# Kernel optimization log

Measured on AMD Instinct MI355X. Metric: run time of the kernel, lower is better.

## Reference

```python
import jax, jax.numpy as jnp
import numpy as np

N, E, IN_DIM, HID, H, D = 50000, 800000, 1280, 256, 4, 64  # gat_out_dim = H*D = HID
NEG_SLOPE = 0.2


def setup_inputs() -> dict:
    key = jax.random.key(0)
    ks = jax.random.split(key, 20)

    def lin(k, fi, fo):
        return (jax.random.normal(k, (fi, fo), jnp.float32) / np.float32(np.sqrt(fi)))

    inp = {
        "x": jax.random.normal(ks[0], (N, IN_DIM), jnp.float32),
        "edge_index": jax.random.randint(ks[1], (2, E), 0, N, dtype=jnp.int32),
        "enc_W": lin(ks[2], IN_DIM, HID), "enc_b": jnp.zeros((HID,), jnp.float32),
        "Wl0": lin(ks[3], HID, H * D), "bl0": jnp.zeros((H * D,), jnp.float32),
        "Wr0": lin(ks[4], HID, H * D), "br0": jnp.zeros((H * D,), jnp.float32),
        "att0": jax.random.normal(ks[5], (H, D), jnp.float32) / np.float32(np.sqrt(D)),
        "bias0": jnp.zeros((H * D,), jnp.float32),
        "Wl1": lin(ks[6], HID, H * D), "bl1": jnp.zeros((H * D,), jnp.float32),
        "Wr1": lin(ks[7], HID, H * D), "br1": jnp.zeros((H * D,), jnp.float32),
        "att1": jax.random.normal(ks[8], (H, D), jnp.float32) / np.float32(np.sqrt(D)),
        "bias1": jnp.zeros((H * D,), jnp.float32),
        "clf_W": lin(ks[9], HID, 1), "clf_b": jnp.zeros((1,), jnp.float32),
    }
    return inp


def gatv2_layer(x, src, dst, Wl, bl, Wr, br, att, bias):
    # x: [N, HID]; src/dst: [E'] with self-loops already appended
    xl = (x @ Wl + bl).reshape(N, H, D)  # source transform
    xr = (x @ Wr + br).reshape(N, H, D)  # target transform
    e = jax.nn.leaky_relu(xl[src] + xr[dst], NEG_SLOPE)   # [E', H, D]
    logits = jnp.einsum('ehd,hd->eh', e, att)              # [E', H]
    # segment softmax over destination nodes (every node has a self-loop)
    m = jax.ops.segment_max(logits, dst, num_segments=N)   # [N, H]
    a = jnp.exp(logits - m[dst])
    denom = jax.ops.segment_sum(a, dst, num_segments=N)
    alpha = a / (denom[dst] + 1e-16)                       # [E', H]
    out = jax.ops.segment_sum(xl[src] * alpha[:, :, None], dst, num_segments=N)
    out = out.reshape(N, H * D) + bias
    out = out + x  # residual (in_dim == out_features -> identity residual); dropout is eval-mode no-op
    return jax.nn.elu(out), alpha


def reference(x, edge_index, enc_W, enc_b, Wl0, bl0, Wr0, br0, att0, bias0,
              Wl1, bl1, Wr1, br1, att1, bias1, clf_W, clf_b):
    # add self loops (PyG GATv2Conv default)
    loops = jnp.arange(N, dtype=edge_index.dtype)
    src = jnp.concatenate([edge_index[0], loops])
    dst = jnp.concatenate([edge_index[1], loops])

    h = x @ enc_W + enc_b                                  # node encoder [N, HID]
    h, alpha0 = gatv2_layer(h, src, dst, Wl0, bl0, Wr0, br0, att0, bias0)
    h, alpha1 = gatv2_layer(h, src, dst, Wl1, bl1, Wr1, br1, att1, bias1)
    preds = (h @ clf_W + clf_b).squeeze(-1)                # [N]
    return preds, alpha0, alpha1
```

## Files before the change

kernel.cpp:

```cpp
#include <hip/hip_runtime.h>
#include <hip/hip_bf16.h>
#include <math.h>

#define N_NODES 50000
#define E_EDGES 800000
#define EP (E_EDGES + N_NODES)
#define IN_DIM 1280
#define HID 256
#define NHEAD 4
#define DHEAD 64
#define NEG_SLOPE 0.2f

typedef unsigned short ushort_t;
typedef __attribute__((ext_vector_type(8))) short short8;
typedef __attribute__((ext_vector_type(4))) float floatx4;

__device__ __forceinline__ void split_bf16(float x, ushort_t& hi, ushort_t& lo) {
  unsigned u = __float_as_uint(x);
  hi = (ushort_t)(u >> 16);
  float rem = x - __uint_as_float(u & 0xFFFF0000u);
  lo = (ushort_t)(__float_as_uint(rem) >> 16);
}

__device__ __forceinline__ void gload_lds16(const void* g, void* l) {
  __builtin_amdgcn_global_load_lds(
      (const __attribute__((address_space(1))) unsigned int*)g,
      (__attribute__((address_space(3))) unsigned int*)l, 16, 0, 0);
}


__global__ void hist_kernel(const int* __restrict__ ei, int* __restrict__ deg) {
  int e = blockIdx.x * blockDim.x + threadIdx.x;
  if (e >= EP) return;
  int dst = (e < E_EDGES) ? ei[E_EDGES + e] : (e - E_EDGES);
  atomicAdd(&deg[dst], 1);
}

__global__ __launch_bounds__(1024) void scan_kernel(int* __restrict__ dc, int* __restrict__ row_ptr) {
  __shared__ int wsum[16];
  int tid = threadIdx.x;
  int lane = tid & 63;
  int wid = tid >> 6;
  int running = 0;
  if (tid == 0) row_ptr[0] = 0;
  for (int base = 0; base < N_NODES; base += 1024) {
    int i = base + tid;
    int v = (i < N_NODES) ? dc[i] : 0;
    int s = v;
    #pragma unroll
    for (int off = 1; off < 64; off <<= 1) {
      int t = __shfl_up(s, off);
      if (lane >= off) s += t;
    }
    if (lane == 63) wsum[wid] = s;
    __syncthreads();
    if (wid == 0 && lane < 16) {
      int w = wsum[lane];
      #pragma unroll
      for (int off = 1; off < 16; off <<= 1) {
        int t = __shfl_up(w, off);
        if (lane >= off) w += t;
      }
      wsum[lane] = w;
    }
    __syncthreads();
    int woff = (wid > 0) ? wsum[wid - 1] : 0;
    int incl = running + woff + s;
    if (i < N_NODES) {
      row_ptr[i + 1] = incl;
      dc[i] = incl - v;
    }
    running += wsum[15];
    __syncthreads();
  }
}

__global__ void scatter_kernel(const int* __restrict__ ei, int* __restrict__ cursor,
                               int2* __restrict__ csr_se) {
  int e = blockIdx.x * blockDim.x + threadIdx.x;
  if (e >= EP) return;
  int src, dst;
  if (e < E_EDGES) { src = ei[e]; dst = ei[E_EDGES + e]; }
  else             { src = dst = e - E_EDGES; }
  int pos = atomicAdd(&cursor[dst], 1);
  csr_se[pos] = make_int2(src, e);
}

#define ENC_ELEMS (IN_DIM * HID)
#define LYR_ELEMS (HID * HID)
__global__ void wsplit_all(const float* __restrict__ enc_W,
                           const float* __restrict__ Wl0, const float* __restrict__ Wr0,
                           const float* __restrict__ Wl1, const float* __restrict__ Wr1,
                           ushort_t* __restrict__ encPh, ushort_t* __restrict__ encPl,
                           ushort_t* __restrict__ P0h, ushort_t* __restrict__ P0l,
                           ushort_t* __restrict__ P1h, ushort_t* __restrict__ P1l) {
  int idx = blockIdx.x * blockDim.x + threadIdx.x;
  const float* W; ushort_t *Ph, *Pl; int NcT, colOff, r;
  if (idx < ENC_ELEMS) {
    W = enc_W; Ph = encPh; Pl = encPl; NcT = HID; colOff = 0; r = idx;
  } else {
    int q = idx - ENC_ELEMS;
    int mId = q >> 16;
    if (mId >= 4) return;
    r = q & 0xFFFF;
    W  = (mId == 0) ? Wl0 : (mId == 1) ? Wr0 : (mId == 2) ? Wl1 : Wr1;
    Ph = (mId < 2) ? P0h : P1h;
    Pl = (mId < 2) ? P0l : P1l;
    NcT = 512; colOff = (mId & 1) * 256;
  }
  int k = r >> 8, n = r & 255;
  ushort_t hi, lo;
  split_bf16(W[r], hi, lo);
  size_t pi = ((size_t)(k >> 3) * NcT + colOff + n) * 8 + (k & 7);
  Ph[pi] = hi;
  Pl[pi] = lo;
}

__device__ __forceinline__ void split_store16(const float* va, ushort_t* dAh,
                                              ushort_t* dAl, int awoff) {
  #pragma unroll
  for (int hh = 0; hh < 2; ++hh) {
    short8 hv, lv;
    #pragma unroll
    for (int i = 0; i < 8; ++i) {
      ushort_t hi, lo;
      split_bf16(va[hh * 8 + i], hi, lo);
      hv[i] = (short)hi; lv[i] = (short)lo;
    }
    *(short8*)&dAh[awoff + hh * 8] = hv;
    *(short8*)&dAl[awoff + hh * 8] = lv;
  }
}

__global__ __launch_bounds__(256, 2) void gemm128(const float* __restrict__ A,
                                                  const ushort_t* __restrict__ Bh,
                                                  const ushort_t* __restrict__ Bl,
                                                  const float* __restrict__ bias_l,
                                                  const float* __restrict__ bias_r,
                                                  float* __restrict__ C_l,
                                                  float* __restrict__ C_r,
                                                  int M, int K, int NcT, int Nsplit) {
  __shared__ ushort_t sAh[2][128 * 40];
  __shared__ ushort_t sAl[2][128 * 40];
  __shared__ ushort_t sBh[2][128 * 32];
  __shared__ ushort_t sBl[2][128 * 32];

  const int P = NcT >> 7;
  const int plog = (P == 2) ? 1 : 2;
  const int id = blockIdx.x;
  const int xcd = id & 7;
  const int kk = id >> 3;
  const int cpan = kk & (P - 1);
  const int Rhi = kk >> plog;
  const int R = (Rhi << 3) + xcd;
  const int MBp = (M + 127) >> 7;
  if (R >= MBp) return;

  const int tid = threadIdx.x;
  const int lane = tid & 63;
  const int w = tid >> 6;
  const int wm = w >> 1, wn = w & 1;
  const int bm = R * 128;
  const int bn = cpan * 128;
  const int r = lane & 15, q = lane >> 4;

  floatx4 acc[4][4];
  #pragma unroll
  for (int i = 0; i < 4; ++i)
    #pragma unroll
    for (int j = 0; j < 4; ++j) acc[i][j] = (floatx4)(0.0f);

  const int arow = tid >> 1, achunk = tid & 1;
  int ag = bm + arow; if (ag >= M) ag = M - 1;
  const float* aptr = A + (size_t)ag * K + achunk * 16;
  const int awoff = arow * 40 + achunk * 16;

  const int e0 = tid, e1 = tid + 256;
  const size_t b0base = ((size_t)(e0 >> 7) * NcT + bn + (e0 & 127)) * 8;
  const size_t b1base = ((size_t)(e1 >> 7) * NcT + bn + (e1 & 127)) * 8;

  const int nt = K >> 5;

  {
    gload_lds16(Bh + b0base, &sBh[0][e0 * 8]);
    gload_lds16(Bh + b1base, &sBh[0][e1 * 8]);
    gload_lds16(Bl + b0base, &sBl[0][e0 * 8]);
    gload_lds16(Bl + b1base, &sBl[0][e1 * 8]);
    float va[16];
    *(float4*)&va[0]  = *(const float4*)(aptr + 0);
    *(float4*)&va[4]  = *(const float4*)(aptr + 4);
    *(float4*)&va[8]  = *(const float4*)(aptr + 8);
    *(float4*)&va[12] = *(const float4*)(aptr + 12);
    split_store16(va, sAh[0], sAl[0], awoff);
  }
  __syncthreads();

  int cur = 0;
  for (int t = 0; t < nt; ++t) {
    const bool has_next = (t + 1 < nt);
    float va[16];
    if (has_next) {
      const int k0n = (t + 1) << 5;
      *(float4*)&va[0]  = *(const float4*)(aptr + k0n + 0);
      *(float4*)&va[4]  = *(const float4*)(aptr + k0n + 4);
      *(float4*)&va[8]  = *(const float4*)(aptr + k0n + 8);
      *(float4*)&va[12] = *(const float4*)(aptr + k0n + 12);
      size_t kadd = (size_t)(k0n >> 3) * NcT * 8;
      gload_lds16(Bh + b0base + kadd, &sBh[cur ^ 1][e0 * 8]);
      gload_lds16(Bh + b1base + kadd, &sBh[cur ^ 1][e1 * 8]);
      gload_lds16(Bl + b0base + kadd, &sBl[cur ^ 1][e0 * 8]);
      gload_lds16(Bl + b1base + kadd, &sBl[cur ^ 1][e1 * 8]);
    }

    short8 ah[4], al[4];
    #pragma unroll
    for (int i = 0; i < 4; ++i) {
      int off = (wm * 64 + i * 16 + r) * 40 + q * 8;
      ah[i] = *(const short8*)&sAh[cur][off];
      al[i] = *(const short8*)&sAl[cur][off];
    }
    #pragma unroll
    for (int j = 0; j < 4; ++j) {
      int off = (q * 128 + wn * 64 + j * 16 + r) * 8;
      short8 bh = *(const short8*)&sBh[cur][off];
      short8 bl = *(const short8*)&sBl[cur][off];
      #pragma unroll
      for (int i = 0; i < 4; ++i) {
        acc[i][j] = __builtin_amdgcn_mfma_f32_16x16x32_bf16(ah[i], bh, acc[i][j], 0, 0, 0);
        acc[i][j] = __builtin_amdgcn_mfma_f32_16x16x32_bf16(ah[i], bl, acc[i][j], 0, 0, 0);
        acc[i][j] = __builtin_amdgcn_mfma_f32_16x16x32_bf16(al[i], bh, acc[i][j], 0, 0, 0);
      }
    }

    if (has_next) split_store16(va, sAh[cur ^ 1], sAl[cur ^ 1], awoff);

    __syncthreads();
    cur ^= 1;
  }

  #pragma unroll
  for (int j = 0; j < 4; ++j) {
    int cg = bn + wn * 64 + j * 16 + r;
    bool sec = cg >= Nsplit;
    int cc = sec ? cg - Nsplit : cg;
    float bv = sec ? bias_r[cc] : bias_l[cc];
    float* Cb = sec ? C_r : C_l;
    #pragma unroll
    for (int i = 0; i < 4; ++i) {
      int row0 = bm + wm * 64 + i * 16 + q * 4;
      #pragma unroll
      for (int rr = 0; rr < 4; ++rr) {
        int row = row0 + rr;
        if (row < M) Cb[(size_t)row * HID + cc] = acc[i][j][rr] + bv;
      }
    }
  }
}

__global__ __launch_bounds__(256) void gat_layer(const float* __restrict__ xl,
                                                 const float* __restrict__ xr,
                                                 float* h_inout,
                                                 const float* __restrict__ att,
                                                 const float* __restrict__ bias,
                                                 const int* __restrict__ row_ptr,
                                                 const int2* __restrict__ csr_se,
                                                 float* __restrict__ logits_ws,
                                                 float* __restrict__ alpha_out,
                                                 const float* __restrict__ clf_W,
                                                 const float* __restrict__ clf_b,
                                                 float* __restrict__ preds) {
  int node = blockIdx.x * 4 + (threadIdx.x >> 6);
  int l = threadIdx.x & 63;
  int hgrp = l >> 4;
  int r0 = row_ptr[node];
  int r1 = row_ptr[node + 1];

  float4 xr4 = *(const float4*)(xr + (size_t)node * HID + l * 4);
  float4 at4 = *(const float4*)(att + l * 4);

  float mA = -INFINITY, mB = -INFINITY;
  float dA = 0.f, dB = 0.f;
  float4 aA = make_float4(0.f, 0.f, 0.f, 0.f);
  float4 aB = make_float4(0.f, 0.f, 0.f, 0.f);

  auto process = [&](const float4& v, int j, float& m, float& den, float4& acc) {
    float t0 = v.x + xr4.x; t0 = (t0 > 0.f) ? t0 : NEG_SLOPE * t0;
    float t1 = v.y + xr4.y; t1 = (t1 > 0.f) ? t1 : NEG_SLOPE * t1;
    float t2 = v.z + xr4.z; t2 = (t2 > 0.f) ? t2 : NEG_SLOPE * t2;
    float t3 = v.w + xr4.w; t3 = (t3 > 0.f) ? t3 : NEG_SLOPE * t3;
    float p = t0 * at4.x + t1 * at4.y + t2 * at4.z + t3 * at4.w;
    p += __shfl_xor(p, 1);
    p += __shfl_xor(p, 2);
    p += __shfl_xor(p, 4);
    p += __shfl_xor(p, 8);
    if ((l & 15) == 0) logits_ws[(size_t)j * NHEAD + hgrp] = p;
    float m_new = fmaxf(m, p);
    float scale = __expf(m - m_new);
    float wgt = __expf(p - m_new);
    den = den * scale + wgt;
    acc.x = acc.x * scale + wgt * v.x;
    acc.y = acc.y * scale + wgt * v.y;
    acc.z = acc.z * scale + wgt * v.z;
    acc.w = acc.w * scale + wgt * v.w;
    m = m_new;
  };

  float4 v0, v1;
  {
    int s0 = csr_se[r0].x;
    int s1 = (r0 + 1 < r1) ? csr_se[r0 + 1].x : s0;
    v0 = *(const float4*)(xl + (size_t)s0 * HID + l * 4);
    v1 = *(const float4*)(xl + (size_t)s1 * HID + l * 4);
  }
  for (int j = r0; j < r1; j += 2) {
    float4 w0 = v0, w1 = v1;
    int jn = j + 2;
    if (jn < r1) {
      int t0 = csr_se[jn].x;
      int t1 = (jn + 1 < r1) ? csr_se[jn + 1].x : t0;
      v0 = *(const float4*)(xl + (size_t)t0 * HID + l * 4);
      v1 = *(const float4*)(xl + (size_t)t1 * HID + l * 4);
    }
    process(w0, j, mA, dA, aA);
    if (j + 1 < r1) process(w1, j + 1, mB, dB, aB);
  }
  float m = fmaxf(mA, mB);
  float e1 = __expf(mA - m);
  float e2 = __expf(mB - m);
  float den = dA * e1 + dB * e2;
  float4 acc;
  acc.x = aA.x * e1 + aB.x * e2;
  acc.y = aA.y * e1 + aB.y * e2;
  acc.z = aA.z * e1 + aB.z * e2;
  acc.w = aA.w * e1 + aB.w * e2;

  float inv_den = 1.f / (den + 1e-16f);

  float4 b4 = *(const float4*)(bias + l * 4);
  float4 h4 = *(const float4*)(h_inout + (size_t)node * HID + l * 4);
  float o0 = acc.x * inv_den + b4.x + h4.x;
  float o1 = acc.y * inv_den + b4.y + h4.y;
  float o2 = acc.z * inv_den + b4.z + h4.z;
  float o3 = acc.w * inv_den + b4.w + h4.w;
  o0 = (o0 > 0.f) ? o0 : (__expf(o0) - 1.f);
  o1 = (o1 > 0.f) ? o1 : (__expf(o1) - 1.f);
  o2 = (o2 > 0.f) ? o2 : (__expf(o2) - 1.f);
  o3 = (o3 > 0.f) ? o3 : (__expf(o3) - 1.f);
  *(float4*)(h_inout + (size_t)node * HID + l * 4) = make_float4(o0, o1, o2, o3);

  if (preds != nullptr) {
    float4 cw = *(const float4*)(clf_W + l * 4);
    float s = o0 * cw.x + o1 * cw.y + o2 * cw.z + o3 * cw.w;
    s += __shfl_xor(s, 1);
    s += __shfl_xor(s, 2);
    s += __shfl_xor(s, 4);
    s += __shfl_xor(s, 8);
    s += __shfl_xor(s, 16);
    s += __shfl_xor(s, 32);
    if (l == 0) preds[node] = s + clf_b[0];
  }

  __threadfence_block();

  float mh = __shfl(m, (l & 3) * 16);
  float dh = __shfl(den, (l & 3) * 16);
  float invd = 1.f / (dh + 1e-16f);
  for (int j = r0 + (l >> 2); j < r1; j += 16) {
    float lg = logits_ws[(size_t)j * NHEAD + (l & 3)];
    alpha_out[(size_t)csr_se[j].y * NHEAD + (l & 3)] = __expf(lg - mh) * invd;
  }
}

static inline char* carve(char*& p, size_t bytes) {
  char* ret = p;
  p += (bytes + 255) & ~(size_t)255;
  return ret;
}

extern "C" void kernel_launch(void* const* d_in, const int* in_sizes, int n_in,
                              void* d_out, int out_size, void* d_ws, size_t ws_size,
                              hipStream_t stream) {
  const float* x     = (const float*)d_in[0];
  const int*   ei    = (const int*)d_in[1];
  const float* enc_W = (const float*)d_in[2];
  const float* enc_b = (const float*)d_in[3];
  const float* Wl0   = (const float*)d_in[4];
  const float* bl0   = (const float*)d_in[5];
  const float* Wr0   = (const float*)d_in[6];
  const float* br0   = (const float*)d_in[7];
  const float* att0  = (const float*)d_in[8];
  const float* bias0 = (const float*)d_in[9];
  const float* Wl1   = (const float*)d_in[10];
  const float* bl1   = (const float*)d_in[11];
  const float* Wr1   = (const float*)d_in[12];
  const float* br1   = (const float*)d_in[13];
  const float* att1  = (const float*)d_in[14];
  const float* bias1 = (const float*)d_in[15];
  const float* clf_W = (const float*)d_in[16];
  const float* clf_b = (const float*)d_in[17];

  float* preds  = (float*)d_out;
  float* alpha0 = preds + N_NODES;
  float* alpha1 = alpha0 + (size_t)EP * NHEAD;

  char* p = (char*)d_ws;
  float* h      = (float*)carve(p, (size_t)N_NODES * HID * 4);
  float* xl     = (float*)carve(p, (size_t)N_NODES * HID * 4);
  float* xr     = (float*)carve(p, (size_t)N_NODES * HID * 4);
  float* logits = (float*)carve(p, (size_t)EP * NHEAD * 4);
  int* row_ptr  = (int*)carve(p, (size_t)(N_NODES + 1) * 4);
  int* cursor   = (int*)carve(p, (size_t)N_NODES * 4);
  int2* csr_se  = (int2*)carve(p, (size_t)EP * 8);
  ushort_t* encPh = (ushort_t*)carve(p, (size_t)IN_DIM * HID * 2);
  ushort_t* encPl = (ushort_t*)carve(p, (size_t)IN_DIM * HID * 2);
  ushort_t* P0h   = (ushort_t*)carve(p, (size_t)HID * 512 * 2);
  ushort_t* P0l   = (ushort_t*)carve(p, (size_t)HID * 512 * 2);
  ushort_t* P1h   = (ushort_t*)carve(p, (size_t)HID * 512 * 2);
  ushort_t* P1l   = (ushort_t*)carve(p, (size_t)HID * 512 * 2);

  hipMemsetAsync(cursor, 0, N_NODES * sizeof(int), stream);
  int eb = 256, eg = (EP + eb - 1) / eb;
  hist_kernel<<<eg, eb, 0, stream>>>(ei, cursor);
  scan_kernel<<<1, 1024, 0, stream>>>(cursor, row_ptr);
  scatter_kernel<<<eg, eb, 0, stream>>>(ei, cursor, csr_se);

  {
    const int total = ENC_ELEMS + 4 * LYR_ELEMS;
    wsplit_all<<<(total + 255) / 256, 256, 0, stream>>>(enc_W, Wl0, Wr0, Wl1, Wr1,
                                                        encPh, encPl, P0h, P0l, P1h, P1l);
  }

  const int MB = (N_NODES + 127) / 128;
  const int R8 = (MB + 7) / 8;
  dim3 bGemm(256);

  gemm128<<<dim3(8 * 2 * R8), bGemm, 0, stream>>>(x, encPh, encPl, enc_b, enc_b, h, h,
                                                  N_NODES, IN_DIM, HID, HID);

  gemm128<<<dim3(8 * 4 * R8), bGemm, 0, stream>>>(h, P0h, P0l, bl0, br0, xl, xr,
                                                  N_NODES, HID, 512, HID);
  gat_layer<<<N_NODES / 4, 256, 0, stream>>>(xl, xr, h, att0, bias0, row_ptr, csr_se,
                                             logits, alpha0, nullptr, nullptr, nullptr);

  gemm128<<<dim3(8 * 4 * R8), bGemm, 0, stream>>>(h, P1h, P1l, bl1, br1, xl, xr,
                                                  N_NODES, HID, 512, HID);
  gat_layer<<<N_NODES / 4, 256, 0, stream>>>(xl, xr, h, att1, bias1, row_ptr, csr_se,
                                             logits, alpha1, clf_W, clf_b, preds);
}
```

Baseline: 1.067 ms.

## Store hidden state pre-split into packed bf16 hi/lo layout for direct LDS loads

The encoder GEMM and the GAT layers now write the hidden state as bf16 hi/lo halves in a K-blocked packed layout padded to MPAD rows. The per-layer GEMMs read it through a new gemm128b kernel that uses direct global-to-LDS loads and skips the in-kernel fp32 split of the A operand. The GAT kernel drops its two interleaved online-softmax accumulators for a single one. The scan kernel now gives each thread a contiguous chunk instead of looping over 1024-wide passes. The costs are scattered 2-byte stores in the GEMM epilogue and a small change in rounding of the residual.

```diff
diff --git a/kernel.cpp b/kernel.cpp
--- a/kernel.cpp
+++ b/kernel.cpp
@@ -10,9 +10,11 @@
 #define NHEAD 4
 #define DHEAD 64
 #define NEG_SLOPE 0.2f
+#define MPAD 50048
 
 typedef unsigned short ushort_t;
 typedef __attribute__((ext_vector_type(8))) short short8;
+typedef __attribute__((ext_vector_type(4))) short short4v;
 typedef __attribute__((ext_vector_type(4))) float floatx4;
 
 __device__ __forceinline__ void split_bf16(float x, ushort_t& hi, ushort_t& lo) {
@@ -22,6 +24,10 @@
   lo = (ushort_t)(__float_as_uint(rem) >> 16);
 }
 
+__device__ __forceinline__ float b2f(short u) {
+  return __uint_as_float(((unsigned)(ushort_t)u) << 16);
+}
+
 __device__ __forceinline__ void gload_lds16(const void* g, void* l) {
   __builtin_amdgcn_global_load_lds(
       (const __attribute__((address_space(1))) unsigned int*)g,
@@ -36,42 +42,51 @@
   atomicAdd(&deg[dst], 1);
 }
 
+#define SCAN_PER 49
 __global__ __launch_bounds__(1024) void scan_kernel(int* __restrict__ dc, int* __restrict__ row_ptr) {
-  __shared__ int wsum[16];
-  int tid = threadIdx.x;
-  int lane = tid & 63;
-  int wid = tid >> 6;
-  int running = 0;
+  __shared__ int wtot[16];
+  const int tid = threadIdx.x;
+  const int lane = tid & 63;
+  const int wid = tid >> 6;
+  const int base = tid * SCAN_PER;
+
+  int v[SCAN_PER];
+  int sum = 0;
+  #pragma unroll
+  for (int k = 0; k < SCAN_PER; ++k) {
+    int i = base + k;
+    int x = (i < N_NODES) ? dc[i] : 0;
+    v[k] = x;
+    sum += x;
+  }
+  int s = sum;
+  #pragma unroll
+  for (int off = 1; off < 64; off <<= 1) {
+    int t = __shfl_up(s, off);
+    if (lane >= off) s += t;
+  }
+  if (lane == 63) wtot[wid] = s;
+  __syncthreads();
+  if (tid < 16) {
+    int w = wtot[tid];
+    #pragma unroll
+    for (int off = 1; off < 16; off <<= 1) {
+      int t = __shfl_up(w, off);
+      if (lane >= off) w += t;
+    }
+    wtot[tid] = w;
+  }
+  __syncthreads();
+  int run = (s - sum) + ((wid > 0) ? wtot[wid - 1] : 0);
   if (tid == 0) row_ptr[0] = 0;
-  for (int base = 0; base < N_NODES; base += 1024) {
-    int i = base + tid;
-    int v = (i < N_NODES) ? dc[i] : 0;
-    int s = v;
-    #pragma unroll
-    for (int off = 1; off < 64; off <<= 1) {
-      int t = __shfl_up(s, off);
-      if (lane >= off) s += t;
-    }
-    if (lane == 63) wsum[wid] = s;
-    __syncthreads();
-    if (wid == 0 && lane < 16) {
-      int w = wsum[lane];
-      #pragma unroll
-      for (int off = 1; off < 16; off <<= 1) {
-        int t = __shfl_up(w, off);
-        if (lane >= off) w += t;
-      }
-      wsum[lane] = w;
-    }
-    __syncthreads();
-    int woff = (wid > 0) ? wsum[wid - 1] : 0;
-    int incl = running + woff + s;
+  #pragma unroll
+  for (int k = 0; k < SCAN_PER; ++k) {
+    int i = base + k;
     if (i < N_NODES) {
-      row_ptr[i + 1] = incl;
-      dc[i] = incl - v;
-    }
-    running += wsum[15];
-    __syncthreads();
+      run += v[k];
+      row_ptr[i + 1] = run;
+      dc[i] = run - v[k];
+    }
   }
 }
 
@@ -139,7 +154,9 @@
                                                   const float* __restrict__ bias_r,
                                                   float* __restrict__ C_l,
                                                   float* __restrict__ C_r,
-                                                  int M, int K, int NcT, int Nsplit) {
+                                                  int M, int K, int NcT, int Nsplit,
+                                                  ushort_t* __restrict__ Ah_out,
+                                                  ushort_t* __restrict__ Al_out) {
   __shared__ ushort_t sAh[2][128 * 40];
   __shared__ ushort_t sAl[2][128 * 40];
   __shared__ ushort_t sBh[2][128 * 32];
@@ -251,6 +268,135 @@
       #pragma unroll
       for (int rr = 0; rr < 4; ++rr) {
         int row = row0 + rr;
+        if (row < M) {
+          float val = acc[i][j][rr] + bv;
+          if (Cb) Cb[(size_t)row * HID + cc] = val;
+          if (Ah_out) {
+            ushort_t hi, lo;
+            split_bf16(val, hi, lo);
+            size_t pidx = ((size_t)(cg >> 3) * MPAD + row) * 8 + (cg & 7);
+            Ah_out[pidx] = hi;
+            Al_out[pidx] = lo;
+          }
+        }
+      }
+    }
+  }
+}
+
+__global__ __launch_bounds__(256, 2) void gemm128b(const ushort_t* __restrict__ Ah,
+                                                   const ushort_t* __restrict__ Al,
+                                                   const ushort_t* __restrict__ Bh,
+                                                   const ushort_t* __restrict__ Bl,
+                                                   const float* __restrict__ bias_l,
+                                                   const float* __restrict__ bias_r,
+                                                   float* __restrict__ C_l,
+                                                   float* __restrict__ C_r,
+                                                   int M, int K, int NcT, int Nsplit) {
+  __shared__ ushort_t sAh[2][128 * 32];
+  __shared__ ushort_t sAl[2][128 * 32];
+  __shared__ ushort_t sBh[2][128 * 32];
+  __shared__ ushort_t sBl[2][128 * 32];
+
+  const int P = NcT >> 7;
+  const int plog = (P == 2) ? 1 : 2;
+  const int id = blockIdx.x;
+  const int xcd = id & 7;
+  const int kk = id >> 3;
+  const int cpan = kk & (P - 1);
+  const int Rhi = kk >> plog;
+  const int R = (Rhi << 3) + xcd;
+  const int MBp = (M + 127) >> 7;
+  if (R >= MBp) return;
+
+  const int tid = threadIdx.x;
+  const int lane = tid & 63;
+  const int w = tid >> 6;
+  const int wm = w >> 1, wn = w & 1;
+  const int bm = R * 128;
+  const int bn = cpan * 128;
+  const int r = lane & 15, q = lane >> 4;
+
+  floatx4 acc[4][4];
+  #pragma unroll
+  for (int i = 0; i < 4; ++i)
+    #pragma unroll
+    for (int j = 0; j < 4; ++j) acc[i][j] = (floatx4)(0.0f);
+
+  const int e0 = tid, e1 = tid + 256;
+  const size_t a0base = ((size_t)(e0 >> 7) * MPAD + bm + (e0 & 127)) * 8;
+  const size_t a1base = ((size_t)(e1 >> 7) * MPAD + bm + (e1 & 127)) * 8;
+  const size_t b0base = ((size_t)(e0 >> 7) * NcT + bn + (e0 & 127)) * 8;
+  const size_t b1base = ((size_t)(e1 >> 7) * NcT + bn + (e1 & 127)) * 8;
+
+  const int nt = K >> 5;
+
+  {
+    gload_lds16(Ah + a0base, &sAh[0][e0 * 8]);
+    gload_lds16(Ah + a1base, &sAh[0][e1 * 8]);
+    gload_lds16(Al + a0base, &sAl[0][e0 * 8]);
+    gload_lds16(Al + a1base, &sAl[0][e1 * 8]);
+    gload_lds16(Bh + b0base, &sBh[0][e0 * 8]);
+    gload_lds16(Bh + b1base, &sBh[0][e1 * 8]);
+    gload_lds16(Bl + b0base, &sBl[0][e0 * 8]);
+    gload_lds16(Bl + b1base, &sBl[0][e1 * 8]);
+  }
+  __syncthreads();
+
+  int cur = 0;
+  for (int t = 0; t < nt; ++t) {
+    const bool has_next = (t + 1 < nt);
+    if (has_next) {
+      const int k0n = (t + 1) << 5;
+      size_t kaddA = (size_t)(k0n >> 3) * MPAD * 8;
+      size_t kaddB = (size_t)(k0n >> 3) * NcT * 8;
+      gload_lds16(Ah + a0base + kaddA, &sAh[cur ^ 1][e0 * 8]);
+      gload_lds16(Ah + a1base + kaddA, &sAh[cur ^ 1][e1 * 8]);
+      gload_lds16(Al + a0base + kaddA, &sAl[cur ^ 1][e0 * 8]);
+      gload_lds16(Al + a1base + kaddA, &sAl[cur ^ 1][e1 * 8]);
+      gload_lds16(Bh + b0base + kaddB, &sBh[cur ^ 1][e0 * 8]);
+      gload_lds16(Bh + b1base + kaddB, &sBh[cur ^ 1][e1 * 8]);
+      gload_lds16(Bl + b0base + kaddB, &sBl[cur ^ 1][e0 * 8]);
+      gload_lds16(Bl + b1base + kaddB, &sBl[cur ^ 1][e1 * 8]);
+    }
+
+    short8 ah[4], al[4];
+    #pragma unroll
+    for (int i = 0; i < 4; ++i) {
+      int off = (q * 128 + wm * 64 + i * 16 + r) * 8;
+      ah[i] = *(const short8*)&sAh[cur][off];
+      al[i] = *(const short8*)&sAl[cur][off];
+    }
+    #pragma unroll
+    for (int j = 0; j < 4; ++j) {
+      int off = (q * 128 + wn * 64 + j * 16 + r) * 8;
+      short8 bh = *(const short8*)&sBh[cur][off];
+      short8 bl = *(const short8*)&sBl[cur][off];
+      #pragma unroll
+      for (int i = 0; i < 4; ++i) {
+        acc[i][j] = __builtin_amdgcn_mfma_f32_16x16x32_bf16(ah[i], bh, acc[i][j], 0, 0, 0);
+        acc[i][j] = __builtin_amdgcn_mfma_f32_16x16x32_bf16(ah[i], bl, acc[i][j], 0, 0, 0);
+        acc[i][j] = __builtin_amdgcn_mfma_f32_16x16x32_bf16(al[i], bh, acc[i][j], 0, 0, 0);
+      }
+    }
+
+    __syncthreads();
+    cur ^= 1;
+  }
+
+  #pragma unroll
+  for (int j = 0; j < 4; ++j) {
+    int cg = bn + wn * 64 + j * 16 + r;
+    bool sec = cg >= Nsplit;
+    int cc = sec ? cg - Nsplit : cg;
+    float bv = sec ? bias_r[cc] : bias_l[cc];
+    float* Cb = sec ? C_r : C_l;
+    #pragma unroll
+    for (int i = 0; i < 4; ++i) {
+      int row0 = bm + wm * 64 + i * 16 + q * 4;
+      #pragma unroll
+      for (int rr = 0; rr < 4; ++rr) {
+        int row = row0 + rr;
         if (row < M) Cb[(size_t)row * HID + cc] = acc[i][j][rr] + bv;
       }
     }
@@ -259,13 +405,15 @@
 
 __global__ __launch_bounds__(256) void gat_layer(const float* __restrict__ xl,
                                                  const float* __restrict__ xr,
-                                                 float* h_inout,
+                                                 ushort_t* __restrict__ hsH,
+                                                 ushort_t* __restrict__ hsL,
                                                  const float* __restrict__ att,
                                                  const float* __restrict__ bias,
                                                  const int* __restrict__ row_ptr,
                                                  const int2* __restrict__ csr_se,
                                                  float* __restrict__ logits_ws,
                                                  float* __restrict__ alpha_out,
+                                                 int writeback,
                                                  const float* __restrict__ clf_W,
                                                  const float* __restrict__ clf_b,
                                                  float* __restrict__ preds) {
@@ -278,12 +426,11 @@
   float4 xr4 = *(const float4*)(xr + (size_t)node * HID + l * 4);
   float4 at4 = *(const float4*)(att + l * 4);
 
-  float mA = -INFINITY, mB = -INFINITY;
-  float dA = 0.f, dB = 0.f;
-  float4 aA = make_float4(0.f, 0.f, 0.f, 0.f);
-  float4 aB = make_float4(0.f, 0.f, 0.f, 0.f);
-
-  auto process = [&](const float4& v, int j, float& m, float& den, float4& acc) {
+  float m = -INFINITY;
+  float den = 0.f;
+  float4 acc = make_float4(0.f, 0.f, 0.f, 0.f);
+
+  auto process = [&](const float4& v, int j) {
     float t0 = v.x + xr4.x; t0 = (t0 > 0.f) ? t0 : NEG_SLOPE * t0;
     float t1 = v.y + xr4.y; t1 = (t1 > 0.f) ? t1 : NEG_SLOPE * t1;
     float t2 = v.z + xr4.z; t2 = (t2 > 0.f) ? t2 : NEG_SLOPE * t2;
@@ -321,32 +468,34 @@
       v0 = *(const float4*)(xl + (size_t)t0 * HID + l * 4);
       v1 = *(const float4*)(xl + (size_t)t1 * HID + l * 4);
     }
-    process(w0, j, mA, dA, aA);
-    if (j + 1 < r1) process(w1, j + 1, mB, dB, aB);
-  }
-  float m = fmaxf(mA, mB);
-  float e1 = __expf(mA - m);
-  float e2 = __expf(mB - m);
-  float den = dA * e1 + dB * e2;
-  float4 acc;
-  acc.x = aA.x * e1 + aB.x * e2;
-  acc.y = aA.y * e1 + aB.y * e2;
-  acc.z = aA.z * e1 + aB.z * e2;
-  acc.w = aA.w * e1 + aB.w * e2;
-
+    process(w0, j);
+    if (j + 1 < r1) process(w1, j + 1);
+  }
   float inv_den = 1.f / (den + 1e-16f);
 
+  const size_t pb = ((size_t)(l >> 1) * MPAD + node) * 8 + ((4 * l) & 7);
+  short4v rh = *(const short4v*)&hsH[pb];
+  short4v rl = *(const short4v*)&hsL[pb];
   float4 b4 = *(const float4*)(bias + l * 4);
-  float4 h4 = *(const float4*)(h_inout + (size_t)node * HID + l * 4);
-  float o0 = acc.x * inv_den + b4.x + h4.x;
-  float o1 = acc.y * inv_den + b4.y + h4.y;
-  float o2 = acc.z * inv_den + b4.z + h4.z;
-  float o3 = acc.w * inv_den + b4.w + h4.w;
+  float o0 = acc.x * inv_den + b4.x + b2f(rh[0]) + b2f(rl[0]);
+  float o1 = acc.y * inv_den + b4.y + b2f(rh[1]) + b2f(rl[1]);
+  float o2 = acc.z * inv_den + b4.z + b2f(rh[2]) + b2f(rl[2]);
+  float o3 = acc.w * inv_den + b4.w + b2f(rh[3]) + b2f(rl[3]);
   o0 = (o0 > 0.f) ? o0 : (__expf(o0) - 1.f);
   o1 = (o1 > 0.f) ? o1 : (__expf(o1) - 1.f);
   o2 = (o2 > 0.f) ? o2 : (__expf(o2) - 1.f);
   o3 = (o3 > 0.f) ? o3 : (__expf(o3) - 1.f);
-  *(float4*)(h_inout + (size_t)node * HID + l * 4) = make_float4(o0, o1, o2, o3);
+
+  if (writeback) {
+    short4v hv, lv;
+    ushort_t hi, lo;
+    split_bf16(o0, hi, lo); hv[0] = (short)hi; lv[0] = (short)lo;
+    split_bf16(o1, hi, lo); hv[1] = (short)hi; lv[1] = (short)lo;
+    split_bf16(o2, hi, lo); hv[2] = (short)hi; lv[2] = (short)lo;
+    split_bf16(o3, hi, lo); hv[3] = (short)hi; lv[3] = (short)lo;
+    *(short4v*)&hsH[pb] = hv;
+    *(short4v*)&hsL[pb] = lv;
+  }
 
   if (preds != nullptr) {
     float4 cw = *(const float4*)(clf_W + l * 4);
@@ -404,7 +553,6 @@
   float* alpha1 = alpha0 + (size_t)EP * NHEAD;
 
   char* p = (char*)d_ws;
-  float* h      = (float*)carve(p, (size_t)N_NODES * HID * 4);
   float* xl     = (float*)carve(p, (size_t)N_NODES * HID * 4);
   float* xr     = (float*)carve(p, (size_t)N_NODES * HID * 4);
   float* logits = (float*)carve(p, (size_t)EP * NHEAD * 4);
@@ -417,6 +565,8 @@
   ushort_t* P0l   = (ushort_t*)carve(p, (size_t)HID * 512 * 2);
   ushort_t* P1h   = (ushort_t*)carve(p, (size_t)HID * 512 * 2);
   ushort_t* P1l   = (ushort_t*)carve(p, (size_t)HID * 512 * 2);
+  ushort_t* hsH   = (ushort_t*)carve(p, (size_t)MPAD * HID * 2);
+  ushort_t* hsL   = (ushort_t*)carve(p, (size_t)MPAD * HID * 2);
 
   hipMemsetAsync(cursor, 0, N_NODES * sizeof(int), stream);
   int eb = 256, eg = (EP + eb - 1) / eb;
@@ -434,16 +584,19 @@
   const int R8 = (MB + 7) / 8;
   dim3 bGemm(256);
 
-  gemm128<<<dim3(8 * 2 * R8), bGemm, 0, stream>>>(x, encPh, encPl, enc_b, enc_b, h, h,
-                                                  N_NODES, IN_DIM, HID, HID);
-
-  gemm128<<<dim3(8 * 4 * R8), bGemm, 0, stream>>>(h, P0h, P0l, bl0, br0, xl, xr,
-                                                  N_NODES, HID, 512, HID);
-  gat_layer<<<N_NODES / 4, 256, 0, stream>>>(xl, xr, h, att0, bias0, row_ptr, csr_se,
-                                             logits, alpha0, nullptr, nullptr, nullptr);
-
-  gemm128<<<dim3(8 * 4 * R8), bGemm, 0, stream>>>(h, P1h, P1l, bl1, br1, xl, xr,
-                                                  N_NODES, HID, 512, HID);
-  gat_layer<<<N_NODES / 4, 256, 0, stream>>>(xl, xr, h, att1, bias1, row_ptr, csr_se,
-                                             logits, alpha1, clf_W, clf_b, preds);
-}
+  gemm128<<<dim3(8 * 2 * R8), bGemm, 0, stream>>>(x, encPh, encPl, enc_b, enc_b,
+                                                  nullptr, nullptr,
+                                                  N_NODES, IN_DIM, HID, HID, hsH, hsL);
+
+  gemm128b<<<dim3(8 * 4 * R8), bGemm, 0, stream>>>(hsH, hsL, P0h, P0l, bl0, br0, xl, xr,
+                                                   N_NODES, HID, 512, HID);
+  gat_layer<<<N_NODES / 4, 256, 0, stream>>>(xl, xr, hsH, hsL, att0, bias0, row_ptr,
+                                             csr_se, logits, alpha0, 1,
+                                             nullptr, nullptr, nullptr);
+
+  gemm128b<<<dim3(8 * 4 * R8), bGemm, 0, stream>>>(hsH, hsL, P1h, P1l, bl1, br1, xl, xr,
+                                                   N_NODES, HID, 512, HID);
+  gat_layer<<<N_NODES / 4, 256, 0, stream>>>(xl, xr, hsH, hsL, att1, bias1, row_ptr,
+                                             csr_se, logits, alpha1, 0,
+                                             clf_W, clf_b, preds);
+}
```

New measurement: 1.157 ms. 8.4% more time.
